# Optimization experiments

Measured on AMD Instinct MI355X. Metric: run time of the kernel, lower is better.

Reference implementation:

```python
import jax, jax.numpy as jnp
import numpy as np

B, C_IN, T = 256, 7, 160
PATCH, D_MODEL, N_LAYERS = 10, 512, 2
D_STATE, D_CONV, EXPAND = 16, 4, 2
L_TOK = T // PATCH            # 16 tokens
D_INNER = EXPAND * D_MODEL    # 1024
DT_RANK = D_MODEL // 16       # 32
EPS = 1e-5


def setup_inputs() -> dict:
    key = jax.random.key(0)
    ks = iter(jax.random.split(key, 32))
    def rn(shape, s=0.02):
        return jax.random.normal(next(ks), shape, dtype=jnp.float32) * s
    return {
        'x': jax.random.normal(next(ks), (B, C_IN, T), dtype=jnp.float32),
        'bn_gamma': jnp.ones((C_IN,), jnp.float32),
        'bn_beta': jnp.zeros((C_IN,), jnp.float32),
        'bn_mean': jnp.zeros((C_IN,), jnp.float32),
        'bn_var': jnp.ones((C_IN,), jnp.float32),
        'patch_w': rn((D_MODEL, C_IN * PATCH)),
        'patch_b': jnp.zeros((D_MODEL,), jnp.float32),
        'ln_patch_g': jnp.ones((D_MODEL,), jnp.float32),
        'ln_patch_b': jnp.zeros((D_MODEL,), jnp.float32),
        'pos': rn((1, L_TOK, D_MODEL)),
        'blk_ln_g': jnp.ones((N_LAYERS, D_MODEL), jnp.float32),
        'blk_ln_b': jnp.zeros((N_LAYERS, D_MODEL), jnp.float32),
        'in_proj_w': rn((N_LAYERS, 2, D_MODEL, 2 * D_INNER)),
        'conv_w': rn((N_LAYERS, 2, D_INNER, D_CONV), 0.1),
        'conv_b': jnp.zeros((N_LAYERS, 2, D_INNER), jnp.float32),
        'x_proj_w': rn((N_LAYERS, 2, D_INNER, DT_RANK + 2 * D_STATE)),
        'dt_proj_w': rn((N_LAYERS, 2, DT_RANK, D_INNER), 0.1),
        'dt_proj_b': jnp.full((N_LAYERS, 2, D_INNER), -4.6, jnp.float32),
        'A_log': jnp.tile(jnp.log(jnp.arange(1, D_STATE + 1, dtype=jnp.float32)), (N_LAYERS, 2, D_INNER, 1)),
        'Dskip': jnp.ones((N_LAYERS, 2, D_INNER), jnp.float32),
        'out_proj_w': rn((N_LAYERS, 2, D_INNER, D_MODEL)),
        'final_ln_g': jnp.ones((D_MODEL,), jnp.float32),
        'final_ln_b': jnp.zeros((D_MODEL,), jnp.float32),
    }


def _ln(x, g, b):
    m = x.mean(-1, keepdims=True)
    v = ((x - m) ** 2).mean(-1, keepdims=True)
    return (x - m) * jax.lax.rsqrt(v + EPS) * g + b


def _mamba_dir(x, Wi, cw, cb, Wx, Wdt, bdt, A_log, Dv, Wo):
    # x: (B, L, d_model) -> (B, L, d_model); one-direction S6 mamba
    u, z = jnp.split(x @ Wi, 2, axis=-1)              # (B,L,D_INNER) each
    Lq = u.shape[1]
    up = jnp.pad(u, ((0, 0), (D_CONV - 1, 0), (0, 0)))  # causal depthwise conv
    uc = cb + sum(up[:, k:k + Lq, :] * cw[:, k] for k in range(D_CONV))
    uc = jax.nn.silu(uc)
    proj = uc @ Wx                                     # (B,L,DT_RANK+2*D_STATE)
    dtr = proj[..., :DT_RANK]
    Bm = proj[..., DT_RANK:DT_RANK + D_STATE]
    Cm = proj[..., DT_RANK + D_STATE:]
    dt = jax.nn.softplus(dtr @ Wdt + bdt)              # (B,L,D_INNER)
    A = -jnp.exp(A_log)                                # (D_INNER,D_STATE)
    dA = jnp.exp(dt[..., None] * A)                    # (B,L,D_INNER,D_STATE)
    dBu = (dt * uc)[..., None] * Bm[:, :, None, :]     # (B,L,D_INNER,D_STATE)

    def step(h, inp):
        dA_t, dBu_t, C_t = inp
        h = dA_t * h + dBu_t                           # (B,D_INNER,D_STATE)
        return h, jnp.einsum('bdn,bn->bd', h, C_t)

    h0 = jnp.zeros((x.shape[0], D_INNER, D_STATE), x.dtype)
    _, ys = jax.lax.scan(step, h0, (dA.swapaxes(0, 1), dBu.swapaxes(0, 1), Cm.swapaxes(0, 1)))
    y = ys.swapaxes(0, 1) + uc * Dv
    return (y * jax.nn.silu(z)) @ Wo


def reference(x, bn_gamma, bn_beta, bn_mean, bn_var, patch_w, patch_b,
              ln_patch_g, ln_patch_b, pos, blk_ln_g, blk_ln_b, in_proj_w,
              conv_w, conv_b, x_proj_w, dt_proj_w, dt_proj_b, A_log, Dskip,
              out_proj_w, final_ln_g, final_ln_b):
    # 1. input BatchNorm1d (eval mode, running stats)
    xn = (x - bn_mean[:, None]) * jax.lax.rsqrt(bn_var[:, None] + EPS) * bn_gamma[:, None] + bn_beta[:, None]
    # 2. patch embed: (B,C,T) -> (B,L,C*PATCH) -> (B,L,d_model)
    p = xn.reshape(B, C_IN, L_TOK, PATCH).transpose(0, 2, 1, 3).reshape(B, L_TOK, C_IN * PATCH)
    h = _ln(p @ patch_w.T + patch_b, ln_patch_g, ln_patch_b)
    # 3. positional embedding
    h = h + pos[:, :L_TOK]
    # 4. Bi-Mamba blocks
    for i in range(N_LAYERS):
        hn = _ln(h, blk_ln_g[i], blk_ln_b[i])
        yf = _mamba_dir(hn, in_proj_w[i, 0], conv_w[i, 0], conv_b[i, 0], x_proj_w[i, 0],
                        dt_proj_w[i, 0], dt_proj_b[i, 0], A_log[i, 0], Dskip[i, 0], out_proj_w[i, 0])
        yb = _mamba_dir(hn[:, ::-1], in_proj_w[i, 1], conv_w[i, 1], conv_b[i, 1], x_proj_w[i, 1],
                        dt_proj_w[i, 1], dt_proj_b[i, 1], A_log[i, 1], Dskip[i, 1], out_proj_w[i, 1])[:, ::-1]
        h = h + yf + yb
    # 5. final LayerNorm
    return _ln(h, final_ln_g, final_ln_b)
```

## Files before the change

kernel.cpp:

```cpp
#include <hip/hip_runtime.h>
#include <math.h>
#include <stdint.h>

#define BB 256
#define C_IN 7
#define TT 160
#define PATCH 10
#define D_MODEL 512
#define L_TOK 16
#define D_INNER 1024
#define D_STATE 16
#define DT_RANK 32
#define EPS 1e-5f
#define NROWS (BB*L_TOK)
#define KPAD 96

typedef __bf16 bf16x8 __attribute__((ext_vector_type(8)));
typedef float  f32x4  __attribute__((ext_vector_type(4)));

__device__ __forceinline__ float siluf(float x){ return x / (1.f + __expf(-x)); }
__device__ __forceinline__ float softplusf(float x){ return (x > 20.f) ? x : log1pf(__expf(x)); }

__device__ __forceinline__ void gload_lds16(const void* gp, void* lp){
  __builtin_amdgcn_global_load_lds(
      (const __attribute__((address_space(1))) unsigned int*)(uintptr_t)gp,
      (__attribute__((address_space(3))) unsigned int*)(uintptr_t)lp, 16, 0, 0);
}

__device__ __forceinline__ float block_reduce_sum(float v, float* sred4){
  for(int off=32; off>0; off>>=1) v += __shfl_down(v, off, 64);
  int lane = threadIdx.x & 63, wid = threadIdx.x >> 6;
  if(lane==0) sred4[wid] = v;
  __syncthreads();
  if(threadIdx.x==0) sred4[0] = sred4[0]+sred4[1]+sred4[2]+sred4[3];
  __syncthreads();
  float r = sred4[0];
  __syncthreads();
  return r;
}

__global__ __launch_bounds__(256) void transpose_bf16_kernel(
    const float* __restrict__ in, __bf16* __restrict__ out, int K, int N)
{
  __shared__ float tile[32][33];
  size_t moff = (size_t)blockIdx.z * K * N;
  int n0 = blockIdx.x*32, k0 = blockIdx.y*32;
  int tx = threadIdx.x, ty = threadIdx.y;
  #pragma unroll
  for(int rr=0;rr<4;rr++)
    tile[ty+rr*8][tx] = in[moff + (size_t)(k0+ty+rr*8)*N + n0+tx];
  __syncthreads();
  #pragma unroll
  for(int rr=0;rr<4;rr++)
    out[moff + (size_t)(n0+ty+rr*8)*K + k0+tx] = (__bf16)tile[tx][ty+rr*8];
}

__global__ __launch_bounds__(256) void transpose_outw_kernel(
    const float* __restrict__ in, __bf16* __restrict__ out)
{
  __shared__ float tile[32][33];
  int z = blockIdx.z, layer = z>>1, dir = z&1;
  int n0 = blockIdx.x*32, k0 = blockIdx.y*32;
  int tx = threadIdx.x, ty = threadIdx.y;
  const float* ip = in + (size_t)z*1024*512;
  #pragma unroll
  for(int rr=0;rr<4;rr++)
    tile[ty+rr*8][tx] = ip[(size_t)(k0+ty+rr*8)*512 + n0+tx];
  __syncthreads();
  __bf16* op = out + (size_t)layer*512*2048 + (size_t)dir*1024;
  #pragma unroll
  for(int rr=0;rr<4;rr++)
    op[(size_t)(n0+ty+rr*8)*2048 + k0+tx] = (__bf16)tile[tx][ty+rr*8];
}

__global__ __launch_bounds__(256) void bn_patchify_kernel(
    const float* __restrict__ x, const float* __restrict__ bng,
    const float* __restrict__ bnb, const float* __restrict__ bnm,
    const float* __restrict__ bnv, __bf16* __restrict__ Abuf)
{
  int idx = blockIdx.x*256 + threadIdx.x;
  int row = idx / KPAD, k = idx % KPAD;
  int b = row >> 4, l = row & 15;
  float v = 0.f;
  if(k < C_IN*PATCH){
    int c = k / PATCH, j = k % PATCH;
    float xv = x[(b*C_IN + c)*TT + l*PATCH + j];
    v = (xv - bnm[c]) * rsqrtf(bnv[c] + EPS) * bng[c] + bnb[c];
  }
  Abuf[idx] = (__bf16)v;
}

__global__ __launch_bounds__(256) void cast_pad_pw_kernel(
    const float* __restrict__ pw, __bf16* __restrict__ pwb)
{
  int idx = blockIdx.x*256 + threadIdx.x;
  if(idx >= 512*KPAD) return;
  int n = idx / KPAD, k = idx % KPAD;
  pwb[idx] = (__bf16)(k < C_IN*PATCH ? pw[n*(C_IN*PATCH) + k] : 0.f);
}

template<int BN, int ACC, int EPI>
__global__ __launch_bounds__(256) void mfma_gemm(
    const __bf16* __restrict__ A, const __bf16* __restrict__ Bt,
    float* __restrict__ C, __bf16* __restrict__ Cb,
    const float* __restrict__ bias, int N, int K, int lda, int ldb,
    size_t sA, size_t sB, size_t sC, size_t sBias)
{
  constexpr int NGB = BN/16;
  constexpr int FN  = BN/32;
  constexpr int BPW = NGB/4;
  __shared__ __align__(16) __bf16 As[8*512];
  __shared__ __align__(16) __bf16 Bs[NGB*512];
  int z = blockIdx.z;
  A  += (size_t)z*sA;  Bt += (size_t)z*sB;  C += (size_t)z*sC;
  if(EPI==1) Cb += (size_t)z*sC;
  if(EPI==2) bias += (size_t)z*sBias;
  int tid  = threadIdx.x;
  int lane = tid & 63, w = tid >> 6;
  int wrow = w >> 1, wcol = w & 1;
  int r = lane & 15, q = lane >> 4;
  int row0 = blockIdx.y*128, col0 = blockIdx.x*BN;

  f32x4 acc[4][FN];
  #pragma unroll
  for(int i=0;i<4;i++)
    #pragma unroll
    for(int j=0;j<FN;j++) acc[i][j] = (f32x4)0.f;

  const __bf16* aSrc[2];
  #pragma unroll
  for(int g2=0;g2<2;g2++)
    aSrc[g2] = A + (size_t)(row0 + (w*2+g2)*16 + r)*lda + q*8;
  const __bf16* bSrc[BPW];
  #pragma unroll
  for(int g2=0;g2<BPW;g2++)
    bSrc[g2] = Bt + (size_t)(col0 + (w*BPW+g2)*16 + r)*ldb + q*8;

  for(int k0=0;k0<K;k0+=32){
    #pragma unroll
    for(int g2=0;g2<2;g2++)
      gload_lds16(aSrc[g2] + k0, As + (w*2+g2)*512);
    #pragma unroll
    for(int g2=0;g2<BPW;g2++)
      gload_lds16(bSrc[g2] + k0, Bs + (w*BPW+g2)*512);
    __syncthreads();
    bf16x8 aF[4], bF[FN];
    #pragma unroll
    for(int i=0;i<4;i++)
      aF[i] = *(const bf16x8*)(As + (wrow*4+i)*512 + lane*8);
    #pragma unroll
    for(int j=0;j<FN;j++)
      bF[j] = *(const bf16x8*)(Bs + (wcol*FN+j)*512 + lane*8);
    #pragma unroll
    for(int i=0;i<4;i++)
      #pragma unroll
      for(int j=0;j<FN;j++)
        acc[i][j] = __builtin_amdgcn_mfma_f32_16x16x32_bf16(aF[i], bF[j], acc[i][j], 0, 0, 0);
    __syncthreads();
  }

  #pragma unroll
  for(int i=0;i<4;i++){
    int m0 = row0 + wrow*64 + i*16 + q*4;
    #pragma unroll
    for(int j=0;j<FN;j++){
      int n = col0 + wcol*(BN/2) + j*16 + r;
      float* cp = C + (size_t)m0*N + n;
      if(EPI==2){
        float bv = bias[n];
        #pragma unroll
        for(int p=0;p<4;p++) cp[(size_t)p*N] = softplusf(acc[i][j][p] + bv);
      } else {
        #pragma unroll
        for(int p=0;p<4;p++){
          float v = ACC ? cp[(size_t)p*N] + acc[i][j][p] : acc[i][j][p];
          cp[(size_t)p*N] = v;
          if(EPI==1) Cb[(size_t)(m0+p)*N + n] = (__bf16)v;
        }
      }
    }
  }
}

__global__ __launch_bounds__(256) void mfma_inproj_conv(
    const __bf16* __restrict__ A, const __bf16* __restrict__ Bt,
    const float* __restrict__ cw, const float* __restrict__ cb,
    float* __restrict__ uc, __bf16* __restrict__ ucb, __bf16* __restrict__ szb)
{
  constexpr int LDA = 512, LDB = 512, K = 512;
  __shared__ __align__(16) __bf16 As[8*512];
  __shared__ __align__(16) __bf16 Bs[8*512];
  int tid  = threadIdx.x;
  int lane = tid & 63, w = tid >> 6;
  int wrow = w >> 1, wcol = w & 1;
  int r = lane & 15, q = lane >> 4;
  int row0 = blockIdx.y*128, col0 = blockIdx.x*128;

  f32x4 acc[4][4];
  #pragma unroll
  for(int i=0;i<4;i++)
    #pragma unroll
    for(int j=0;j<4;j++) acc[i][j] = (f32x4)0.f;

  const __bf16* aSrc[2];
  #pragma unroll
  for(int g2=0;g2<2;g2++)
    aSrc[g2] = A + (size_t)(row0 + (w*2+g2)*16 + r)*LDA + q*8;
  const __bf16* bSrc[2];
  #pragma unroll
  for(int g2=0;g2<2;g2++)
    bSrc[g2] = Bt + (size_t)(col0 + (w*2+g2)*16 + r)*LDB + q*8;

  for(int k0=0;k0<K;k0+=32){
    #pragma unroll
    for(int g2=0;g2<2;g2++)
      gload_lds16(aSrc[g2] + k0, As + (w*2+g2)*512);
    #pragma unroll
    for(int g2=0;g2<2;g2++)
      gload_lds16(bSrc[g2] + k0, Bs + (w*2+g2)*512);
    __syncthreads();
    bf16x8 aF[4], bF[4];
    #pragma unroll
    for(int i=0;i<4;i++)
      aF[i] = *(const bf16x8*)(As + (wrow*4+i)*512 + lane*8);
    #pragma unroll
    for(int j=0;j<4;j++)
      bF[j] = *(const bf16x8*)(Bs + (wcol*4+j)*512 + lane*8);
    #pragma unroll
    for(int i=0;i<4;i++)
      #pragma unroll
      for(int j=0;j<4;j++)
        acc[i][j] = __builtin_amdgcn_mfma_f32_16x16x32_bf16(aF[i], bF[j], acc[i][j], 0, 0, 0);
    __syncthreads();
  }

  int dirq = col0 >> 11;
  bool is_u = (col0 & 2047) < 1024;
  int dbase = (col0 & 1023) + wcol*64;
  const float* cwd = cw + dirq*4096;
  const float* cbd = cb + dirq*1024;
  float*  ucD  = uc  + (size_t)dirq*NROWS*1024;
  __bf16* ucbD = ucb + (size_t)dirq*NROWS*1024;
  __bf16* szD  = szb + (size_t)dirq*NROWS*1024;

  #pragma unroll
  for(int i=0;i<4;i++){
    int seq = row0 + wrow*64 + i*16;
    #pragma unroll
    for(int j=0;j<4;j++){
      int dloc = dbase + j*16 + r;
      float A0=acc[i][j][0], A1=acc[i][j][1], A2=acc[i][j][2], A3=acc[i][j][3];
      if(is_u){
        float4 w4 = ((const float4*)cwd)[dloc];
        float bv = cbd[dloc];
        float cur[4]={A0,A1,A2,A3};
        float vout[4];
        if(dirq==0){
          float S1=__shfl_up(A1,16,64), S2=__shfl_up(A2,16,64), S3=__shfl_up(A3,16,64);
          float um1[4]={S3,A0,A1,A2};
          float um2[4]={S2,S3,A0,A1};
          float um3[4]={S1,S2,S3,A0};
          #pragma unroll
          for(int p=0;p<4;p++){
            int t=q*4+p;
            float v = bv + w4.w*cur[p];
            v += (t>=1)? w4.z*um1[p] : 0.f;
            v += (t>=2)? w4.y*um2[p] : 0.f;
            v += (t>=3)? w4.x*um3[p] : 0.f;
            vout[p]=v;
          }
        } else {
          float D0=__shfl_down(A0,16,64), D1=__shfl_down(A1,16,64), D2=__shfl_down(A2,16,64);
          float up1[4]={A1,A2,A3,D0};
          float up2[4]={A2,A3,D0,D1};
          float up3[4]={A3,D0,D1,D2};
          #pragma unroll
          for(int p=0;p<4;p++){
            int t=q*4+p;
            float v = bv + w4.w*cur[p];
            v += (t<=14)? w4.z*up1[p] : 0.f;
            v += (t<=13)? w4.y*up2[p] : 0.f;
            v += (t<=12)? w4.x*up3[p] : 0.f;
            vout[p]=v;
          }
        }
        #pragma unroll
        for(int p=0;p<4;p++){
          float s = siluf(vout[p]);
          size_t o = (size_t)(seq + q*4+p)*1024 + dloc;
          ucD[o] = s; ucbD[o] = (__bf16)s;
        }
      } else {
        #pragma unroll
        for(int p=0;p<4;p++)
          szD[(size_t)(seq + q*4+p)*1024 + dloc] = (__bf16)siluf(acc[i][j][p]);
      }
    }
  }
}

__global__ __launch_bounds__(256) void ln_pos_kernel(
    const float* __restrict__ in, const float* __restrict__ pb,
    const float* __restrict__ g, const float* __restrict__ bt,
    const float* __restrict__ pos, float* __restrict__ out)
{
  __shared__ float sred[4];
  int row = blockIdx.x; int l = row & 15; int tid = threadIdx.x;
  const float* ip = in + (size_t)row*512;
  float v0 = ip[tid] + pb[tid], v1 = ip[tid+256] + pb[tid+256];
  float s = block_reduce_sum(v0+v1, sred);
  float mean = s * (1.f/512.f);
  float d0 = v0-mean, d1 = v1-mean;
  float vs = block_reduce_sum(d0*d0+d1*d1, sred);
  float rstd = rsqrtf(vs*(1.f/512.f) + EPS);
  out[(size_t)row*512+tid]     = d0*rstd*g[tid]     + bt[tid]     + pos[l*512+tid];
  out[(size_t)row*512+tid+256] = d1*rstd*g[tid+256] + bt[tid+256] + pos[l*512+tid+256];
}

__global__ __launch_bounds__(256) void ln_bf16_kernel(
    const float* __restrict__ in, const float* __restrict__ g,
    const float* __restrict__ bt, __bf16* __restrict__ out)
{
  __shared__ float sred[4];
  int row = blockIdx.x; int tid = threadIdx.x;
  const float* ip = in + (size_t)row*512;
  float v0 = ip[tid], v1 = ip[tid+256];
  float s = block_reduce_sum(v0+v1, sred);
  float mean = s * (1.f/512.f);
  float d0 = v0-mean, d1 = v1-mean;
  float vs = block_reduce_sum(d0*d0+d1*d1, sred);
  float rstd = rsqrtf(vs*(1.f/512.f) + EPS);
  out[(size_t)row*512+tid]     = (__bf16)(d0*rstd*g[tid]     + bt[tid]);
  out[(size_t)row*512+tid+256] = (__bf16)(d1*rstd*g[tid+256] + bt[tid+256]);
}

__global__ __launch_bounds__(256) void ln_f32_kernel(
    const float* __restrict__ in, const float* __restrict__ g,
    const float* __restrict__ bt, float* __restrict__ out)
{
  __shared__ float sred[4];
  int row = blockIdx.x; int tid = threadIdx.x;
  const float* ip = in + (size_t)row*512;
  float v0 = ip[tid], v1 = ip[tid+256];
  float s = block_reduce_sum(v0+v1, sred);
  float mean = s * (1.f/512.f);
  float d0 = v0-mean, d1 = v1-mean;
  float vs = block_reduce_sum(d0*d0+d1*d1, sred);
  float rstd = rsqrtf(vs*(1.f/512.f) + EPS);
  out[(size_t)row*512+tid]     = d0*rstd*g[tid]     + bt[tid];
  out[(size_t)row*512+tid+256] = d1*rstd*g[tid+256] + bt[tid+256];
}

__global__ __launch_bounds__(256) void scan_kernel(
    const float* __restrict__ dtb, const float* __restrict__ uc,
    const float* __restrict__ proj, const __bf16* __restrict__ szb,
    const float* __restrict__ A_log, const float* __restrict__ Dskip,
    __bf16* __restrict__ gb)
{
  int b = blockIdx.x;
  int dirq = blockIdx.y >> 2;
  int d = (blockIdx.y & 3)*256 + threadIdx.x;
  const float*  dtp = dtb  + (size_t)dirq*NROWS*1024;
  const float*  ucp = uc   + (size_t)dirq*NROWS*1024;
  const float*  prp = proj + (size_t)dirq*NROWS*64;
  const __bf16* szp = szb  + (size_t)dirq*NROWS*1024;
  const float*  Alp = A_log + (size_t)dirq*1024*16;
  float Dv = Dskip[dirq*1024 + d];
  __shared__ float sB[16][16], sC[16][16];
  {
    int s = threadIdx.x >> 4, n = threadIdx.x & 15;
    int tok = dirq ? 15-s : s;
    sB[s][n] = prp[(size_t)(b*16+tok)*64 + 32 + n];
    sC[s][n] = prp[(size_t)(b*16+tok)*64 + 48 + n];
  }
  __syncthreads();
  float a[16], hst[16];
  #pragma unroll
  for(int n=0;n<16;n++){ a[n] = -__expf(Alp[d*16+n]); hst[n]=0.f; }
  for(int s=0;s<16;s++){
    int tok = dirq ? 15-s : s;
    size_t o = (size_t)(b*16+tok)*1024 + d;
    float dtv = dtp[o];
    float ucv = ucp[o];
    float dtu = dtv*ucv;
    float y = 0.f;
    #pragma unroll
    for(int n=0;n<16;n++){
      hst[n] = __expf(dtv*a[n])*hst[n] + dtu*sB[s][n];
      y += hst[n]*sC[s][n];
    }
    float zs = (float)szp[o];
    gb[(size_t)(b*16+tok)*2048 + dirq*1024 + d] = (__bf16)((y + ucv*Dv) * zs);
  }
}

extern "C" void kernel_launch(void* const* d_in, const int* in_sizes, int n_in,
                              void* d_out, int out_size, void* d_ws, size_t ws_size,
                              hipStream_t stream) {
  (void)in_sizes; (void)n_in; (void)out_size; (void)ws_size;
  const float* x         = (const float*)d_in[0];
  const float* bn_gamma  = (const float*)d_in[1];
  const float* bn_beta   = (const float*)d_in[2];
  const float* bn_mean   = (const float*)d_in[3];
  const float* bn_var    = (const float*)d_in[4];
  const float* patch_w   = (const float*)d_in[5];
  const float* patch_b   = (const float*)d_in[6];
  const float* ln_pg     = (const float*)d_in[7];
  const float* ln_pb     = (const float*)d_in[8];
  const float* pos       = (const float*)d_in[9];
  const float* blk_ln_g  = (const float*)d_in[10];
  const float* blk_ln_b  = (const float*)d_in[11];
  const float* in_proj_w = (const float*)d_in[12];
  const float* conv_w    = (const float*)d_in[13];
  const float* conv_b    = (const float*)d_in[14];
  const float* x_proj_w  = (const float*)d_in[15];
  const float* dt_proj_w = (const float*)d_in[16];
  const float* dt_proj_b = (const float*)d_in[17];
  const float* A_log     = (const float*)d_in[18];
  const float* Dskip     = (const float*)d_in[19];
  const float* out_proj_w= (const float*)d_in[20];
  const float* fin_g     = (const float*)d_in[21];
  const float* fin_b     = (const float*)d_in[22];

  char* p = (char*)d_ws;
  float*  h    = (float*)p;  p += (size_t)NROWS*512*4;
  float*  uc2  = (float*)p;  p += (size_t)2*NROWS*1024*4;
  float*  dtb2 = (float*)p;  p += (size_t)2*NROWS*1024*4;
  float*  proj2= (float*)p;  p += (size_t)2*NROWS*64*4;
  __bf16* hnb  = (__bf16*)p; p += (size_t)NROWS*512*2;
  __bf16* ucb2 = (__bf16*)p; p += (size_t)2*NROWS*1024*2;
  __bf16* szb2 = (__bf16*)p; p += (size_t)2*NROWS*1024*2;
  __bf16* gbK  = (__bf16*)p; p += (size_t)NROWS*2048*2;
  __bf16* projb2=(__bf16*)p; p += (size_t)2*NROWS*64*2;
  __bf16* wtin = (__bf16*)p; p += (size_t)4*2048*512*2;
  __bf16* wtoutK=(__bf16*)p; p += (size_t)2*512*2048*2;
  __bf16* wtx  = (__bf16*)p; p += (size_t)4*64*1024*2;
  __bf16* wdtT = (__bf16*)p; p += (size_t)4*1024*32*2;
  __bf16* Abuf = (__bf16*)p; p += (size_t)NROWS*KPAD*2;
  __bf16* pwb  = (__bf16*)p; p += (size_t)512*KPAD*2;

  transpose_bf16_kernel<<<dim3(64, 16, 4), dim3(32,8), 0, stream>>>(
      in_proj_w, wtin, 512, 2048);
  transpose_outw_kernel<<<dim3(16, 32, 4), dim3(32,8), 0, stream>>>(
      out_proj_w, wtoutK);
  transpose_bf16_kernel<<<dim3(2, 32, 4), dim3(32,8), 0, stream>>>(
      x_proj_w, wtx, 1024, 64);
  transpose_bf16_kernel<<<dim3(32, 1, 4), dim3(32,8), 0, stream>>>(
      dt_proj_w, wdtT, 32, 1024);
  cast_pad_pw_kernel<<<(512*KPAD + 255)/256, 256, 0, stream>>>(patch_w, pwb);

  bn_patchify_kernel<<<(NROWS*KPAD)/256, 256, 0, stream>>>(
      x, bn_gamma, bn_beta, bn_mean, bn_var, Abuf);
  mfma_gemm<128,0,0><<<dim3(4, 32, 1), 256, 0, stream>>>(
      Abuf, pwb, dtb2, nullptr, nullptr, 512, KPAD, KPAD, KPAD, 0,0,0,0);
  ln_pos_kernel<<<NROWS, 256, 0, stream>>>(dtb2, patch_b, ln_pg, ln_pb, pos, h);

  for(int i=0;i<2;i++){
    ln_bf16_kernel<<<NROWS, 256, 0, stream>>>(h, blk_ln_g + i*512, blk_ln_b + i*512, hnb);
    mfma_inproj_conv<<<dim3(32, 32), 256, 0, stream>>>(
        hnb, wtin + (size_t)i*4096*512, conv_w + (size_t)i*2*4096,
        conv_b + (size_t)i*2*1024, uc2, ucb2, szb2);
    mfma_gemm<64,0,1><<<dim3(1, 32, 2), 256, 0, stream>>>(
        ucb2, wtx + (size_t)i*2*64*1024, proj2, projb2, nullptr,
        64, 1024, 1024, 1024,
        (size_t)NROWS*1024, (size_t)64*1024, (size_t)NROWS*64, 0);
    mfma_gemm<128,0,2><<<dim3(8, 32, 2), 256, 0, stream>>>(
        projb2, wdtT + (size_t)i*2*1024*32, dtb2, nullptr, dt_proj_b + (size_t)i*2*1024,
        1024, 32, 64, 32,
        (size_t)NROWS*64, (size_t)1024*32, (size_t)NROWS*1024, 1024);
    scan_kernel<<<dim3(BB, 8), 256, 0, stream>>>(
        dtb2, uc2, proj2, szb2, A_log + (size_t)i*2*1024*16,
        Dskip + (size_t)i*2*1024, gbK);
    mfma_gemm<64,1,0><<<dim3(8, 32, 1), 256, 0, stream>>>(
        gbK, wtoutK + (size_t)i*512*2048, h, nullptr, nullptr,
        512, 2048, 2048, 2048, 0,0,0,0);
  }
  ln_f32_kernel<<<NROWS, 256, 0, stream>>>(h, fin_g, fin_b, (float*)d_out);
}
```

Before: 560.5 us.

## Store dt and conv activations in bf16, swap MFMA operands for vectorized epilogues

The conv output and dt activations now stay in bf16 only, which drops the fp32 copies and halves the bytes the scan kernel reads. The MFMA operand order is swapped so each lane holds four consecutive columns, letting epilogues write vector stores and letting the causal conv shift along rows with lane shuffles. GEMM tiles are parameterized by BM/BN/BK with two K-slices per barrier, smaller tiles are used for several launches, and conv weights are staged in LDS. Keeping dt and u in bf16 before the scan lowers precision.

```diff
diff --git a/kernel.cpp b/kernel.cpp
--- a/kernel.cpp
+++ b/kernel.cpp
@@ -16,6 +16,7 @@
 #define KPAD 96
 
 typedef __bf16 bf16x8 __attribute__((ext_vector_type(8)));
+typedef __bf16 bf16x4 __attribute__((ext_vector_type(4)));
 typedef float  f32x4  __attribute__((ext_vector_type(4)));
 
 __device__ __forceinline__ float siluf(float x){ return x / (1.f + __expf(-x)); }
@@ -99,83 +100,100 @@
   pwb[idx] = (__bf16)(k < C_IN*PATCH ? pw[n*(C_IN*PATCH) + k] : 0.f);
 }
 
-template<int BN, int ACC, int EPI>
+template<int BM, int BN, int BK, int ACC, int EPI>
 __global__ __launch_bounds__(256) void mfma_gemm(
     const __bf16* __restrict__ A, const __bf16* __restrict__ Bt,
     float* __restrict__ C, __bf16* __restrict__ Cb,
     const float* __restrict__ bias, int N, int K, int lda, int ldb,
     size_t sA, size_t sB, size_t sC, size_t sBias)
 {
-  constexpr int NGB = BN/16;
-  constexpr int FN  = BN/32;
-  constexpr int BPW = NGB/4;
-  __shared__ __align__(16) __bf16 As[8*512];
-  __shared__ __align__(16) __bf16 Bs[NGB*512];
+  constexpr int NGA = BM/16, NGB = BN/16;
+  constexpr int APW = NGA/4, BPW = NGB/4;
+  constexpr int MI  = BM/32, FN  = BN/32;
+  constexpr int NSL = BK/32;
+  __shared__ __align__(16) __bf16 As[NSL*NGA*512];
+  __shared__ __align__(16) __bf16 Bs[NSL*NGB*512];
   int z = blockIdx.z;
-  A  += (size_t)z*sA;  Bt += (size_t)z*sB;  C += (size_t)z*sC;
-  if(EPI==1) Cb += (size_t)z*sC;
+  A  += (size_t)z*sA;  Bt += (size_t)z*sB;
+  if(EPI!=2) C += (size_t)z*sC;
+  if(EPI!=0) Cb += (size_t)z*sC;
   if(EPI==2) bias += (size_t)z*sBias;
   int tid  = threadIdx.x;
   int lane = tid & 63, w = tid >> 6;
   int wrow = w >> 1, wcol = w & 1;
   int r = lane & 15, q = lane >> 4;
-  int row0 = blockIdx.y*128, col0 = blockIdx.x*BN;
-
-  f32x4 acc[4][FN];
-  #pragma unroll
-  for(int i=0;i<4;i++)
+  int row0 = blockIdx.y*BM, col0 = blockIdx.x*BN;
+
+  f32x4 acc[MI][FN];
+  #pragma unroll
+  for(int i=0;i<MI;i++)
     #pragma unroll
     for(int j=0;j<FN;j++) acc[i][j] = (f32x4)0.f;
 
-  const __bf16* aSrc[2];
-  #pragma unroll
-  for(int g2=0;g2<2;g2++)
-    aSrc[g2] = A + (size_t)(row0 + (w*2+g2)*16 + r)*lda + q*8;
+  const __bf16* aSrc[APW];
+  #pragma unroll
+  for(int g=0;g<APW;g++)
+    aSrc[g] = A + (size_t)(row0 + (w*APW+g)*16 + r)*lda + q*8;
   const __bf16* bSrc[BPW];
   #pragma unroll
-  for(int g2=0;g2<BPW;g2++)
-    bSrc[g2] = Bt + (size_t)(col0 + (w*BPW+g2)*16 + r)*ldb + q*8;
-
-  for(int k0=0;k0<K;k0+=32){
-    #pragma unroll
-    for(int g2=0;g2<2;g2++)
-      gload_lds16(aSrc[g2] + k0, As + (w*2+g2)*512);
-    #pragma unroll
-    for(int g2=0;g2<BPW;g2++)
-      gload_lds16(bSrc[g2] + k0, Bs + (w*BPW+g2)*512);
+  for(int g=0;g<BPW;g++)
+    bSrc[g] = Bt + (size_t)(col0 + (w*BPW+g)*16 + r)*ldb + q*8;
+
+  for(int k0=0;k0<K;k0+=BK){
+    #pragma unroll
+    for(int s=0;s<NSL;s++){
+      #pragma unroll
+      for(int g=0;g<APW;g++)
+        gload_lds16(aSrc[g] + k0 + s*32, As + (s*NGA + w*APW+g)*512);
+      #pragma unroll
+      for(int g=0;g<BPW;g++)
+        gload_lds16(bSrc[g] + k0 + s*32, Bs + (s*NGB + w*BPW+g)*512);
+    }
     __syncthreads();
-    bf16x8 aF[4], bF[FN];
-    #pragma unroll
-    for(int i=0;i<4;i++)
-      aF[i] = *(const bf16x8*)(As + (wrow*4+i)*512 + lane*8);
-    #pragma unroll
-    for(int j=0;j<FN;j++)
-      bF[j] = *(const bf16x8*)(Bs + (wcol*FN+j)*512 + lane*8);
-    #pragma unroll
-    for(int i=0;i<4;i++)
+    #pragma unroll
+    for(int s=0;s<NSL;s++){
+      bf16x8 aF[MI], bF[FN];
+      #pragma unroll
+      for(int i=0;i<MI;i++)
+        aF[i] = *(const bf16x8*)(As + (s*NGA + wrow*MI+i)*512 + lane*8);
       #pragma unroll
       for(int j=0;j<FN;j++)
-        acc[i][j] = __builtin_amdgcn_mfma_f32_16x16x32_bf16(aF[i], bF[j], acc[i][j], 0, 0, 0);
+        bF[j] = *(const bf16x8*)(Bs + (s*NGB + wcol*FN+j)*512 + lane*8);
+      #pragma unroll
+      for(int i=0;i<MI;i++)
+        #pragma unroll
+        for(int j=0;j<FN;j++)
+          acc[i][j] = __builtin_amdgcn_mfma_f32_16x16x32_bf16(bF[j], aF[i], acc[i][j], 0, 0, 0);
+    }
     __syncthreads();
   }
 
   #pragma unroll
-  for(int i=0;i<4;i++){
-    int m0 = row0 + wrow*64 + i*16 + q*4;
+  for(int i=0;i<MI;i++){
+    int m = row0 + wrow*(BM/2) + i*16 + r;
     #pragma unroll
     for(int j=0;j<FN;j++){
-      int n = col0 + wcol*(BN/2) + j*16 + r;
-      float* cp = C + (size_t)m0*N + n;
+      int n = col0 + wcol*(BN/2) + j*16 + q*4;
       if(EPI==2){
-        float bv = bias[n];
+        const float* bp = bias + n;
+        bf16x4 hv;
         #pragma unroll
-        for(int p=0;p<4;p++) cp[(size_t)p*N] = softplusf(acc[i][j][p] + bv);
+        for(int p=0;p<4;p++) hv[p] = (__bf16)softplusf(acc[i][j][p] + bp[p]);
+        *(bf16x4*)(Cb + (size_t)m*N + n) = hv;
       } else {
-        #pragma unroll
-        for(int p=0;p<4;p++){
-          float v = ACC ? cp[(size_t)p*N] + acc[i][j][p] : acc[i][j][p];
-          cp[(size_t)p*N] = v;
-          if(EPI==1) Cb[(size_t)(m0+p)*N + n] = (__bf16)v;
+        float* cp = C + (size_t)m*N + n;
+        f32x4 ov = acc[i][j];
+        if(ACC){
+          f32x4 cv = *(const f32x4*)cp;
+          #pragma unroll
+          for(int p=0;p<4;p++) ov[p] += cv[p];
+        }
+        *(f32x4*)cp = ov;
+        if(EPI==1){
+          bf16x4 hv;
+          #pragma unroll
+          for(int p=0;p<4;p++) hv[p] = (__bf16)ov[p];
+          *(bf16x4*)(Cb + (size_t)m*N + n) = hv;
         }
       }
     }
@@ -185,115 +203,126 @@
 __global__ __launch_bounds__(256) void mfma_inproj_conv(
     const __bf16* __restrict__ A, const __bf16* __restrict__ Bt,
     const float* __restrict__ cw, const float* __restrict__ cb,
-    float* __restrict__ uc, __bf16* __restrict__ ucb, __bf16* __restrict__ szb)
+    __bf16* __restrict__ ucb, __bf16* __restrict__ szb)
 {
   constexpr int LDA = 512, LDB = 512, K = 512;
-  __shared__ __align__(16) __bf16 As[8*512];
-  __shared__ __align__(16) __bf16 Bs[8*512];
+  __shared__ __align__(16) __bf16 As[2*8*512];
+  __shared__ __align__(16) __bf16 Bs[2*8*512];
+  __shared__ float4 s_w4[128];
+  __shared__ float  s_b[128];
   int tid  = threadIdx.x;
   int lane = tid & 63, w = tid >> 6;
   int wrow = w >> 1, wcol = w & 1;
   int r = lane & 15, q = lane >> 4;
   int row0 = blockIdx.y*128, col0 = blockIdx.x*128;
 
-  f32x4 acc[4][4];
-  #pragma unroll
-  for(int i=0;i<4;i++)
-    #pragma unroll
-    for(int j=0;j<4;j++) acc[i][j] = (f32x4)0.f;
-
-  const __bf16* aSrc[2];
-  #pragma unroll
-  for(int g2=0;g2<2;g2++)
-    aSrc[g2] = A + (size_t)(row0 + (w*2+g2)*16 + r)*LDA + q*8;
-  const __bf16* bSrc[2];
-  #pragma unroll
-  for(int g2=0;g2<2;g2++)
-    bSrc[g2] = Bt + (size_t)(col0 + (w*2+g2)*16 + r)*LDB + q*8;
-
-  for(int k0=0;k0<K;k0+=32){
-    #pragma unroll
-    for(int g2=0;g2<2;g2++)
-      gload_lds16(aSrc[g2] + k0, As + (w*2+g2)*512);
-    #pragma unroll
-    for(int g2=0;g2<2;g2++)
-      gload_lds16(bSrc[g2] + k0, Bs + (w*2+g2)*512);
-    __syncthreads();
-    bf16x8 aF[4], bF[4];
-    #pragma unroll
-    for(int i=0;i<4;i++)
-      aF[i] = *(const bf16x8*)(As + (wrow*4+i)*512 + lane*8);
-    #pragma unroll
-    for(int j=0;j<4;j++)
-      bF[j] = *(const bf16x8*)(Bs + (wcol*4+j)*512 + lane*8);
-    #pragma unroll
-    for(int i=0;i<4;i++)
-      #pragma unroll
-      for(int j=0;j<4;j++)
-        acc[i][j] = __builtin_amdgcn_mfma_f32_16x16x32_bf16(aF[i], bF[j], acc[i][j], 0, 0, 0);
-    __syncthreads();
-  }
-
   int dirq = col0 >> 11;
-  bool is_u = (col0 & 2047) < 1024;
-  int dbase = (col0 & 1023) + wcol*64;
+  int feat0 = col0 & 2047;
+  bool is_u = feat0 < 1024;
+  int dblk = col0 & 1023;
   const float* cwd = cw + dirq*4096;
   const float* cbd = cb + dirq*1024;
-  float*  ucD  = uc  + (size_t)dirq*NROWS*1024;
+  if(is_u && tid < 128){
+    s_w4[tid] = ((const float4*)cwd)[dblk + tid];
+    s_b[tid]  = cbd[dblk + tid];
+  }
+
+  f32x4 acc[4][4];
+  #pragma unroll
+  for(int i=0;i<4;i++)
+    #pragma unroll
+    for(int j=0;j<4;j++) acc[i][j] = (f32x4)0.f;
+
+  const __bf16* aSrc[2];
+  #pragma unroll
+  for(int g=0;g<2;g++)
+    aSrc[g] = A + (size_t)(row0 + (w*2+g)*16 + r)*LDA + q*8;
+  const __bf16* bSrc[2];
+  #pragma unroll
+  for(int g=0;g<2;g++)
+    bSrc[g] = Bt + (size_t)(col0 + (w*2+g)*16 + r)*LDB + q*8;
+
+  for(int k0=0;k0<K;k0+=64){
+    #pragma unroll
+    for(int s=0;s<2;s++){
+      #pragma unroll
+      for(int g=0;g<2;g++)
+        gload_lds16(aSrc[g] + k0 + s*32, As + (s*8 + w*2+g)*512);
+      #pragma unroll
+      for(int g=0;g<2;g++)
+        gload_lds16(bSrc[g] + k0 + s*32, Bs + (s*8 + w*2+g)*512);
+    }
+    __syncthreads();
+    #pragma unroll
+    for(int s=0;s<2;s++){
+      bf16x8 aF[4], bF[4];
+      #pragma unroll
+      for(int i=0;i<4;i++)
+        aF[i] = *(const bf16x8*)(As + (s*8 + wrow*4+i)*512 + lane*8);
+      #pragma unroll
+      for(int j=0;j<4;j++)
+        bF[j] = *(const bf16x8*)(Bs + (s*8 + wcol*4+j)*512 + lane*8);
+      #pragma unroll
+      for(int i=0;i<4;i++)
+        #pragma unroll
+        for(int j=0;j<4;j++)
+          acc[i][j] = __builtin_amdgcn_mfma_f32_16x16x32_bf16(bF[j], aF[i], acc[i][j], 0, 0, 0);
+    }
+    __syncthreads();
+  }
+
   __bf16* ucbD = ucb + (size_t)dirq*NROWS*1024;
   __bf16* szD  = szb + (size_t)dirq*NROWS*1024;
 
   #pragma unroll
   for(int i=0;i<4;i++){
-    int seq = row0 + wrow*64 + i*16;
+    int tok = row0 + wrow*64 + i*16 + r;
     #pragma unroll
     for(int j=0;j<4;j++){
-      int dloc = dbase + j*16 + r;
-      float A0=acc[i][j][0], A1=acc[i][j][1], A2=acc[i][j][2], A3=acc[i][j][3];
+      int nloc = wcol*64 + j*16 + q*4;
       if(is_u){
-        float4 w4 = ((const float4*)cwd)[dloc];
-        float bv = cbd[dloc];
-        float cur[4]={A0,A1,A2,A3};
+        int f = nloc;
+        int d = dblk + f;
         float vout[4];
         if(dirq==0){
-          float S1=__shfl_up(A1,16,64), S2=__shfl_up(A2,16,64), S3=__shfl_up(A3,16,64);
-          float um1[4]={S3,A0,A1,A2};
-          float um2[4]={S2,S3,A0,A1};
-          float um3[4]={S1,S2,S3,A0};
           #pragma unroll
           for(int p=0;p<4;p++){
-            int t=q*4+p;
-            float v = bv + w4.w*cur[p];
-            v += (t>=1)? w4.z*um1[p] : 0.f;
-            v += (t>=2)? w4.y*um2[p] : 0.f;
-            v += (t>=3)? w4.x*um3[p] : 0.f;
-            vout[p]=v;
+            float cur = acc[i][j][p];
+            float m1 = __shfl_up(cur, 1, 64);
+            float m2 = __shfl_up(cur, 2, 64);
+            float m3 = __shfl_up(cur, 3, 64);
+            float4 w4 = s_w4[f+p];
+            float v = s_b[f+p] + w4.w*cur;
+            v += (r>=1)? w4.z*m1 : 0.f;
+            v += (r>=2)? w4.y*m2 : 0.f;
+            v += (r>=3)? w4.x*m3 : 0.f;
+            vout[p] = v;
           }
         } else {
-          float D0=__shfl_down(A0,16,64), D1=__shfl_down(A1,16,64), D2=__shfl_down(A2,16,64);
-          float up1[4]={A1,A2,A3,D0};
-          float up2[4]={A2,A3,D0,D1};
-          float up3[4]={A3,D0,D1,D2};
           #pragma unroll
           for(int p=0;p<4;p++){
-            int t=q*4+p;
-            float v = bv + w4.w*cur[p];
-            v += (t<=14)? w4.z*up1[p] : 0.f;
-            v += (t<=13)? w4.y*up2[p] : 0.f;
-            v += (t<=12)? w4.x*up3[p] : 0.f;
-            vout[p]=v;
+            float cur = acc[i][j][p];
+            float p1 = __shfl_down(cur, 1, 64);
+            float p2 = __shfl_down(cur, 2, 64);
+            float p3 = __shfl_down(cur, 3, 64);
+            float4 w4 = s_w4[f+p];
+            float v = s_b[f+p] + w4.w*cur;
+            v += (r<=14)? w4.z*p1 : 0.f;
+            v += (r<=13)? w4.y*p2 : 0.f;
+            v += (r<=12)? w4.x*p3 : 0.f;
+            vout[p] = v;
           }
         }
+        bf16x4 hv;
         #pragma unroll
-        for(int p=0;p<4;p++){
-          float s = siluf(vout[p]);
-          size_t o = (size_t)(seq + q*4+p)*1024 + dloc;
-          ucD[o] = s; ucbD[o] = (__bf16)s;
-        }
+        for(int p=0;p<4;p++) hv[p] = (__bf16)siluf(vout[p]);
+        *(bf16x4*)(ucbD + (size_t)tok*1024 + d) = hv;
       } else {
+        int dz = feat0 - 1024 + nloc;
+        bf16x4 hv;
         #pragma unroll
-        for(int p=0;p<4;p++)
-          szD[(size_t)(seq + q*4+p)*1024 + dloc] = (__bf16)siluf(acc[i][j][p]);
+        for(int p=0;p<4;p++) hv[p] = (__bf16)siluf(acc[i][j][p]);
+        *(bf16x4*)(szD + (size_t)tok*1024 + dz) = hv;
       }
     }
   }
@@ -352,7 +381,7 @@
 }
 
 __global__ __launch_bounds__(256) void scan_kernel(
-    const float* __restrict__ dtb, const float* __restrict__ uc,
+    const __bf16* __restrict__ dtb, const __bf16* __restrict__ ucb,
     const float* __restrict__ proj, const __bf16* __restrict__ szb,
     const float* __restrict__ A_log, const float* __restrict__ Dskip,
     __bf16* __restrict__ gb)
@@ -360,8 +389,8 @@
   int b = blockIdx.x;
   int dirq = blockIdx.y >> 2;
   int d = (blockIdx.y & 3)*256 + threadIdx.x;
-  const float*  dtp = dtb  + (size_t)dirq*NROWS*1024;
-  const float*  ucp = uc   + (size_t)dirq*NROWS*1024;
+  const __bf16* dtp = dtb + (size_t)dirq*NROWS*1024;
+  const __bf16* ucp = ucb + (size_t)dirq*NROWS*1024;
   const float*  prp = proj + (size_t)dirq*NROWS*64;
   const __bf16* szp = szb  + (size_t)dirq*NROWS*1024;
   const float*  Alp = A_log + (size_t)dirq*1024*16;
@@ -380,8 +409,8 @@
   for(int s=0;s<16;s++){
     int tok = dirq ? 15-s : s;
     size_t o = (size_t)(b*16+tok)*1024 + d;
-    float dtv = dtp[o];
-    float ucv = ucp[o];
+    float dtv = (float)dtp[o];
+    float ucv = (float)ucp[o];
     float dtu = dtv*ucv;
     float y = 0.f;
     #pragma unroll
@@ -424,12 +453,11 @@
 
   char* p = (char*)d_ws;
   float*  h    = (float*)p;  p += (size_t)NROWS*512*4;
-  float*  uc2  = (float*)p;  p += (size_t)2*NROWS*1024*4;
-  float*  dtb2 = (float*)p;  p += (size_t)2*NROWS*1024*4;
   float*  proj2= (float*)p;  p += (size_t)2*NROWS*64*4;
   __bf16* hnb  = (__bf16*)p; p += (size_t)NROWS*512*2;
   __bf16* ucb2 = (__bf16*)p; p += (size_t)2*NROWS*1024*2;
   __bf16* szb2 = (__bf16*)p; p += (size_t)2*NROWS*1024*2;
+  __bf16* dtb2 = (__bf16*)p; p += (size_t)2*NROWS*1024*2;
   __bf16* gbK  = (__bf16*)p; p += (size_t)NROWS*2048*2;
   __bf16* projb2=(__bf16*)p; p += (size_t)2*NROWS*64*2;
   __bf16* wtin = (__bf16*)p; p += (size_t)4*2048*512*2;
@@ -451,27 +479,27 @@
 
   bn_patchify_kernel<<<(NROWS*KPAD)/256, 256, 0, stream>>>(
       x, bn_gamma, bn_beta, bn_mean, bn_var, Abuf);
-  mfma_gemm<128,0,0><<<dim3(4, 32, 1), 256, 0, stream>>>(
-      Abuf, pwb, dtb2, nullptr, nullptr, 512, KPAD, KPAD, KPAD, 0,0,0,0);
-  ln_pos_kernel<<<NROWS, 256, 0, stream>>>(dtb2, patch_b, ln_pg, ln_pb, pos, h);
+  mfma_gemm<128,128,32,0,0><<<dim3(4, 32, 1), 256, 0, stream>>>(
+      Abuf, pwb, (float*)gbK, nullptr, nullptr, 512, KPAD, KPAD, KPAD, 0,0,0,0);
+  ln_pos_kernel<<<NROWS, 256, 0, stream>>>((float*)gbK, patch_b, ln_pg, ln_pb, pos, h);
 
   for(int i=0;i<2;i++){
     ln_bf16_kernel<<<NROWS, 256, 0, stream>>>(h, blk_ln_g + i*512, blk_ln_b + i*512, hnb);
     mfma_inproj_conv<<<dim3(32, 32), 256, 0, stream>>>(
         hnb, wtin + (size_t)i*4096*512, conv_w + (size_t)i*2*4096,
-        conv_b + (size_t)i*2*1024, uc2, ucb2, szb2);
-    mfma_gemm<64,0,1><<<dim3(1, 32, 2), 256, 0, stream>>>(
+        conv_b + (size_t)i*2*1024, ucb2, szb2);
+    mfma_gemm<64,64,64,0,1><<<dim3(1, 64, 2), 256, 0, stream>>>(
         ucb2, wtx + (size_t)i*2*64*1024, proj2, projb2, nullptr,
         64, 1024, 1024, 1024,
         (size_t)NROWS*1024, (size_t)64*1024, (size_t)NROWS*64, 0);
-    mfma_gemm<128,0,2><<<dim3(8, 32, 2), 256, 0, stream>>>(
-        projb2, wdtT + (size_t)i*2*1024*32, dtb2, nullptr, dt_proj_b + (size_t)i*2*1024,
+    mfma_gemm<64,64,32,0,2><<<dim3(16, 64, 2), 256, 0, stream>>>(
+        projb2, wdtT + (size_t)i*2*1024*32, nullptr, dtb2, dt_proj_b + (size_t)i*2*1024,
         1024, 32, 64, 32,
         (size_t)NROWS*64, (size_t)1024*32, (size_t)NROWS*1024, 1024);
     scan_kernel<<<dim3(BB, 8), 256, 0, stream>>>(
-        dtb2, uc2, proj2, szb2, A_log + (size_t)i*2*1024*16,
+        dtb2, ucb2, proj2, szb2, A_log + (size_t)i*2*1024*16,
         Dskip + (size_t)i*2*1024, gbK);
-    mfma_gemm<64,1,0><<<dim3(8, 32, 1), 256, 0, stream>>>(
+    mfma_gemm<64,64,64,1,0><<<dim3(8, 64, 1), 256, 0, stream>>>(
         gbK, wtoutK + (size_t)i*512*2048, h, nullptr, nullptr,
         512, 2048, 2048, 2048, 0,0,0,0);
   }
```

After: 497.3 us. 11.3% less time.
